# Optimization experiments

Hardware: AMD Instinct MI355X
Metric: run time of the kernel (lower is better)

The kernel has to match this reference:

```python
import jax, jax.numpy as jnp
import numpy as np

B, S, H, D = 2, 2048, 2048, 256  # batch, seq, hidden, head_dim
NH, NKV = 8, 1                   # attention heads, kv heads
N_REP = NH // NKV
SCALING = D ** -0.5
ROPE_THETA = 10000.0
NEG_INF = -1e9


def rotate_half(x):
    x1, x2 = jnp.split(x, 2, axis=-1)
    return jnp.concatenate((-x2, x1), axis=-1)


def setup_inputs() -> dict:
    key = jax.random.key(0)
    ks = jax.random.split(key, 5)
    hidden_states = jax.random.normal(ks[0], (B, S, H), dtype=jnp.float32)
    # RoPE cos/sin per position, Gemma-style: inv_freq tiled over full head_dim
    inv_freq = 1.0 / (ROPE_THETA ** (np.arange(0, D, 2, dtype=np.float32) / D))  # [D/2]
    pos = np.arange(S, dtype=np.float32)
    freqs = np.outer(pos, inv_freq)                      # [S, D/2]
    emb = np.concatenate([freqs, freqs], axis=-1)        # [S, D]
    cos = jnp.broadcast_to(jnp.asarray(np.cos(emb)), (B, S, D))
    sin = jnp.broadcast_to(jnp.asarray(np.sin(emb)), (B, S, D))
    # additive causal mask [B, 1, S, S]
    causal = jnp.triu(jnp.full((S, S), NEG_INF, dtype=jnp.float32), k=1)
    attention_mask = jnp.broadcast_to(causal[None, None], (B, 1, S, S))
    scale = 0.02
    Wq = jax.random.normal(ks[1], (H, NH * D), dtype=jnp.float32) * scale
    Wk = jax.random.normal(ks[2], (H, NKV * D), dtype=jnp.float32) * scale
    Wv = jax.random.normal(ks[3], (H, NKV * D), dtype=jnp.float32) * scale
    Wo = jax.random.normal(ks[4], (NH * D, H), dtype=jnp.float32) * scale
    return {"hidden_states": hidden_states, "cos": cos, "sin": sin,
            "attention_mask": attention_mask, "Wq": Wq, "Wk": Wk, "Wv": Wv, "Wo": Wo}


def reference(hidden_states, cos, sin, attention_mask, Wq, Wk, Wv, Wo):
    # projections: [B,S,H] @ [H, nh*D] -> [B, nh, S, D]
    q = (hidden_states @ Wq).reshape(B, S, NH, D).transpose(0, 2, 1, 3)
    k = (hidden_states @ Wk).reshape(B, S, NKV, D).transpose(0, 2, 1, 3)
    v = (hidden_states @ Wv).reshape(B, S, NKV, D).transpose(0, 2, 1, 3)
    # RoPE (cos/sin broadcast over head dim via unsqueeze at axis 1)
    c = cos[:, None]  # [B,1,S,D]
    s = sin[:, None]
    q = q * c + rotate_half(q) * s
    k = k * c + rotate_half(k) * s
    # repeat_kv: [B, NKV, S, D] -> [B, NH, S, D]
    k = jnp.repeat(k, N_REP, axis=1)
    v = jnp.repeat(v, N_REP, axis=1)
    # eager attention
    attn_weights = jnp.einsum("bhqd,bhkd->bhqk", q, k) * SCALING
    attn_weights = attn_weights + attention_mask[:, :, :, :S]
    attn_weights = jax.nn.softmax(attn_weights.astype(jnp.float32), axis=-1).astype(q.dtype)
    attn_output = jnp.einsum("bhqk,bhkd->bhqd", attn_weights, v)
    attn_output = attn_output.transpose(0, 2, 1, 3).reshape(B, S, NH * D)
    attn_output = attn_output @ Wo
    return attn_output, attn_weights
```

## Files before the change

### kernel.cpp

```cpp
#include <hip/hip_runtime.h>
#include <hip/hip_bf16.h>

#define B_   2
#define S_   2048
#define H_   2048
#define D_   256
#define NH_  8

typedef unsigned short u16;
typedef __bf16 bf16x8 __attribute__((ext_vector_type(8)));
typedef float f32x4 __attribute__((ext_vector_type(4)));
typedef unsigned int uint4v __attribute__((ext_vector_type(4)));
typedef unsigned int uint2v __attribute__((ext_vector_type(2)));

#define AS1 __attribute__((address_space(1)))
#define AS3 __attribute__((address_space(3)))

__device__ __forceinline__ u16 f2bf(float x) {
  union { float f; unsigned u; } v; v.f = x;
  unsigned u = v.u;
  u += 0x7FFFu + ((u >> 16) & 1u);
  return (u16)(u >> 16);
}
__device__ __forceinline__ float bf2f(u16 x) {
  union { unsigned u; float f; } v; v.u = ((unsigned)x) << 16;
  return v.f;
}

__device__ __forceinline__ void bf8_unpack(uint4v u, float* f) {
  f[0] = bf2f(u.x & 0xffff); f[1] = bf2f(u.x >> 16);
  f[2] = bf2f(u.y & 0xffff); f[3] = bf2f(u.y >> 16);
  f[4] = bf2f(u.z & 0xffff); f[5] = bf2f(u.z >> 16);
  f[6] = bf2f(u.w & 0xffff); f[7] = bf2f(u.w >> 16);
}
__device__ __forceinline__ uint4v bf8_pack(const float* f) {
  uint4v o;
  o.x = (unsigned)f2bf(f[0]) | ((unsigned)f2bf(f[1]) << 16);
  o.y = (unsigned)f2bf(f[2]) | ((unsigned)f2bf(f[3]) << 16);
  o.z = (unsigned)f2bf(f[4]) | ((unsigned)f2bf(f[5]) << 16);
  o.w = (unsigned)f2bf(f[6]) | ((unsigned)f2bf(f[7]) << 16);
  return o;
}

__device__ __forceinline__ void gld_lds16(const u16* g, u16* l) {
  __builtin_amdgcn_global_load_lds((const AS1 unsigned int*)g,
                                   (AS3 unsigned int*)l, 16, 0, 0);
}

#define BM 128
#define BN 128
#define BK 64

enum GemmMode { MODE_PROJ = 0, MODE_QK = 1, MODE_PV = 2, MODE_WO = 3 };

template <int MODE>
__global__ __launch_bounds__(256)
void gemm_nt(const u16* __restrict__ A, const u16* __restrict__ Bb,
             void* __restrict__ Cp, float* __restrict__ rows,
             float* __restrict__ Pout,
             int K, int lda, int ldb, int ldc)
{
  int bn, bm;
  if constexpr (MODE == MODE_QK) {
    int t = blockIdx.x;
    bm = 0;
    while ((bm + 1) * (bm + 2) / 2 <= t) bm++;
    bn = t - bm * (bm + 1) / 2;
  } else if constexpr (MODE == MODE_PV) {
    bn = blockIdx.x;
    bm = (int)gridDim.y - 1 - (int)blockIdx.y;
  } else {
    bn = blockIdx.x;
    bm = blockIdx.y;
  }
  const int bz = blockIdx.z;
  const int m0 = bm * BM, n0 = bn * BN;
  const int tid = threadIdx.x;

  const u16* Ap = A;
  const u16* Bp = Bb;
  float* Cf = (float*)Cp;
  u16*   Cu = (u16*)Cp;
  float* Pp = Pout;

  if constexpr (MODE == MODE_QK) {
    Ap   += (size_t)bz * S_ * D_;
    Bp   += (size_t)(bz >> 3) * S_ * D_;
    Cu   += (size_t)bz * S_ * S_;
    rows += (size_t)bz * S_;
  } else if constexpr (MODE == MODE_PV) {
    Ap   += (size_t)bz * S_ * S_;
    Bp   += (size_t)(bz >> 3) * D_ * S_;
    Cu   += (size_t)(bz >> 3) * S_ * (NH_ * D_) + (size_t)(bz & 7) * D_;
    rows += (size_t)bz * S_;
    Pp   += (size_t)bz * S_ * S_;
  }

  int Keff = K;
  if constexpr (MODE == MODE_PV) {
    int lim = (bm + 1) * BM;
    Keff = lim < K ? lim : K;
  }

  __shared__ __align__(16) u16 smem[BM * BK + BN * BK + 512];
  u16* As = smem;
  u16* Bs = smem + BM * BK;
  __shared__ float invs[BM];

  const int lane = tid & 63;
  const int quad = lane >> 4;
  const int l16  = lane & 15;
  const int wave = tid >> 6;
  const int wm   = (wave >> 1) << 6;
  const int wn   = (wave & 1) << 6;

  if constexpr (MODE == MODE_PV) {
    if (tid < BM) invs[tid] = 1.0f / rows[m0 + tid];
  }

  f32x4 acc[4][4] = {};

  for (int kt = 0; kt < Keff; kt += BK) {
    #pragma unroll
    for (int i = 0; i < 4; i++) {
      int c = tid + i * 256;
      gld_lds16(Ap + (size_t)(m0 + (c >> 3)) * lda + kt + (c & 7) * 8, &As[c * 8]);
    }
    #pragma unroll
    for (int i = 0; i < 4; i++) {
      int c = tid + i * 256;
      gld_lds16(Bp + (size_t)(n0 + (c >> 3)) * ldb + kt + (c & 7) * 8, &Bs[c * 8]);
    }
    __syncthreads();

    #pragma unroll
    for (int kk = 0; kk < 2; kk++) {
      bf16x8 af[4], bfr[4];
      #pragma unroll
      for (int i = 0; i < 4; i++)
        af[i] = *(const bf16x8*)(&As[(wm + i * 16 + l16) * BK + kk * 32 + quad * 8]);
      #pragma unroll
      for (int j = 0; j < 4; j++)
        bfr[j] = *(const bf16x8*)(&Bs[(wn + j * 16 + l16) * BK + kk * 32 + quad * 8]);
      #pragma unroll
      for (int i = 0; i < 4; i++)
        #pragma unroll
        for (int j = 0; j < 4; j++)
          acc[i][j] = __builtin_amdgcn_mfma_f32_16x16x32_bf16(af[i], bfr[j], acc[i][j], 0, 0, 0);
    }

    if constexpr (MODE == MODE_PV) {
      if (bn == 0) {
        const int pr4 = tid >> 4;
        const int pc4 = (tid & 15) * 4;
        #pragma unroll
        for (int rr = 0; rr < BM; rr += 16) {
          const int r = rr + pr4;
          const u16* e = &As[r * BK + pc4];
          const float inv = invs[r];
          float4 o;
          o.x = bf2f(e[0]) * inv; o.y = bf2f(e[1]) * inv;
          o.z = bf2f(e[2]) * inv; o.w = bf2f(e[3]) * inv;
          *(float4*)(Pp + (size_t)(m0 + r) * S_ + kt + pc4) = o;
        }
      }
    }
    __syncthreads();
  }

  if constexpr (MODE == MODE_PV) {
    if (bn == 0 && Keff < S_) {
      const int r8 = tid >> 3;
      const int c8 = tid & 7;
      const float4 z = {0.f, 0.f, 0.f, 0.f};
      #pragma unroll
      for (int rr = 0; rr < BM; rr += 32) {
        float* pr = Pp + (size_t)(m0 + rr + r8) * S_;
        for (int c4 = (Keff >> 2) + c8; c4 < (S_ >> 2); c4 += 8)
          *(float4*)(pr + c4 * 4) = z;
      }
    }
  }

  const float SCL2 = 0.0625f * 1.44269504088896340736f;
  if constexpr (MODE == MODE_WO) {
    float (*Cs32)[132] = (float (*)[132])smem;
    const int band16 = (wave >> 1) * 16;
    #pragma unroll
    for (int i = 0; i < 4; i++) {
      #pragma unroll
      for (int r = 0; r < 4; r++) {
        const int lr = band16 + quad * 4 + r;
        #pragma unroll
        for (int j = 0; j < 4; j++)
          Cs32[lr][wn + j * 16 + l16] = acc[i][j][r];
      }
      __syncthreads();
      #pragma unroll
      for (int ch = tid; ch < 1024; ch += 256) {
        const int rr = ch >> 5, cc = ch & 31;
        const int mg = m0 + ((rr >> 4) << 6) + i * 16 + (rr & 15);
        *(float4*)(Cf + (size_t)mg * ldc + n0 + cc * 4) =
            *(const float4*)(&Cs32[rr][cc * 4]);
      }
      __syncthreads();
    }
  } else {
    u16 (*Cs)[136] = (u16 (*)[136])smem;
    const int band16 = (wave >> 1) * 16;
    #pragma unroll
    for (int i = 0; i < 4; i++) {
      #pragma unroll
      for (int r = 0; r < 4; r++) {
        const int lr = band16 + quad * 4 + r;
        const int m  = m0 + wm + i * 16 + quad * 4 + r;
        if constexpr (MODE == MODE_QK) {
          float rs = 0.f;
          #pragma unroll
          for (int j = 0; j < 4; j++) {
            int n = n0 + wn + j * 16 + l16;
            float e = (n <= m) ? exp2f(acc[i][j][r] * SCL2) : 0.f;
            rs += e;
            Cs[lr][wn + j * 16 + l16] = f2bf(e);
          }
          #pragma unroll
          for (int o = 1; o < 16; o <<= 1) rs += __shfl_xor(rs, o, 64);
          if (l16 == 0) atomicAdd(&rows[m], rs);
        } else if constexpr (MODE == MODE_PV) {
          const float inv = invs[wm + i * 16 + quad * 4 + r];
          #pragma unroll
          for (int j = 0; j < 4; j++)
            Cs[lr][wn + j * 16 + l16] = f2bf(acc[i][j][r] * inv);
        } else {
          #pragma unroll
          for (int j = 0; j < 4; j++)
            Cs[lr][wn + j * 16 + l16] = f2bf(acc[i][j][r]);
        }
      }
      __syncthreads();
      #pragma unroll
      for (int ch = tid; ch < 512; ch += 256) {
        const int rr = ch >> 4, cc = ch & 15;
        const int mg = m0 + ((rr >> 4) << 6) + i * 16 + (rr & 15);
        *(uint4v*)(Cu + (size_t)mg * ldc + n0 + cc * 8) =
            *(const uint4v*)(&Cs[rr][cc * 8]);
      }
      __syncthreads();
    }
  }
}

__device__ __forceinline__ void tc_tile(const float* __restrict__ src,
                                        u16* __restrict__ dst, int K, int N,
                                        int n0, int k0, float (*t)[33])
{
  int c = threadIdx.x & 31, r = threadIdx.x >> 5;
  #pragma unroll
  for (int rr = 0; rr < 32; rr += 8)
    t[r + rr][c] = src[(size_t)(k0 + r + rr) * N + n0 + c];
  __syncthreads();
  #pragma unroll
  for (int rr = 0; rr < 32; rr += 8)
    dst[(size_t)(n0 + r + rr) * K + k0 + c] = f2bf(t[c][r + rr]);
}

__global__ __launch_bounds__(256)
void prep_kernel(const float* __restrict__ X,
                 const float* __restrict__ Wq, const float* __restrict__ Wk,
                 const float* __restrict__ Wv, const float* __restrict__ Wo,
                 u16* __restrict__ Xbf, u16* __restrict__ WT,
                 u16* __restrict__ WoT, float* __restrict__ Rows)
{
  __shared__ float t[32][33];
  const int bid = blockIdx.x;
  if (bid < 4096) {
    tc_tile(Wq, WT, 2048, 2048, (bid & 63) * 32, (bid >> 6) * 32, t);
  } else if (bid < 4608) {
    int l = bid - 4096;
    tc_tile(Wk, WT + 2048 * 2048, 2048, 256, (l & 7) * 32, (l >> 3) * 32, t);
  } else if (bid < 5120) {
    int l = bid - 4608;
    tc_tile(Wv, WT + 2304 * 2048, 2048, 256, (l & 7) * 32, (l >> 3) * 32, t);
  } else if (bid < 9216) {
    int l = bid - 5120;
    tc_tile(Wo, WoT, 2048, 2048, (l & 63) * 32, (l >> 6) * 32, t);
  } else if (bid < 11264) {
    int l = bid - 9216;
    #pragma unroll
    for (int it = 0; it < 4; ++it) {
      int i = it * 524288 + l * 256 + threadIdx.x;
      float4 f = ((const float4*)X)[i];
      uint2v p;
      p.x = (unsigned)f2bf(f.x) | ((unsigned)f2bf(f.y) << 16);
      p.y = (unsigned)f2bf(f.z) | ((unsigned)f2bf(f.w) << 16);
      ((uint2v*)Xbf)[i] = p;
    }
  } else {
    int l = bid - 11264;
    const float4 z = {0.f, 0.f, 0.f, 0.f};
    #pragma unroll
    for (int it = 0; it < 4; ++it)
      ((float4*)Rows)[it * 2048 + l * 256 + threadIdx.x] = z;
  }
}

__global__ __launch_bounds__(256)
void postproj_kernel(const u16* __restrict__ raw, const float* __restrict__ cosb,
                     const float* __restrict__ sinb, u16* __restrict__ qout,
                     u16* __restrict__ kout, u16* __restrict__ vt)
{
  __shared__ u16 t[32][34];
  const int bid = blockIdx.x;
  if (bid < 1024) {
    const int row = threadIdx.x >> 4;
    const int d8  = (threadIdx.x & 15) * 8;
    #pragma unroll
    for (int it2 = 0; it2 < 2; ++it2) {
      int idx = bid * 32 + it2 * 16 + row;
      int h = idx & 7, bs = idx >> 3;
      int b = bs >> 11, s = bs & (S_ - 1);
      size_t base = (size_t)bs * 2560 + (size_t)h * D_;
      uint4v u1 = *(const uint4v*)(raw + base + d8);
      uint4v u2 = *(const uint4v*)(raw + base + 128 + d8);
      float4 c0 = *(const float4*)(cosb + (size_t)bs * D_ + d8);
      float4 c1 = *(const float4*)(cosb + (size_t)bs * D_ + d8 + 4);
      float4 s0 = *(const float4*)(sinb + (size_t)bs * D_ + d8);
      float4 s1 = *(const float4*)(sinb + (size_t)bs * D_ + d8 + 4);
      float a[8], bq[8], cc[8], ss[8], r1[8], r2[8];
      bf8_unpack(u1, a); bf8_unpack(u2, bq);
      cc[0]=c0.x; cc[1]=c0.y; cc[2]=c0.z; cc[3]=c0.w;
      cc[4]=c1.x; cc[5]=c1.y; cc[6]=c1.z; cc[7]=c1.w;
      ss[0]=s0.x; ss[1]=s0.y; ss[2]=s0.z; ss[3]=s0.w;
      ss[4]=s1.x; ss[5]=s1.y; ss[6]=s1.z; ss[7]=s1.w;
      #pragma unroll
      for (int i = 0; i < 8; ++i) {
        r1[i] = a[i] * cc[i] - bq[i] * ss[i];
        r2[i] = bq[i] * cc[i] + a[i] * ss[i];
      }
      size_t ob = (((size_t)b * NH_ + h) * S_ + s) * D_;
      *(uint4v*)(qout + ob + d8)       = bf8_pack(r1);
      *(uint4v*)(qout + ob + 128 + d8) = bf8_pack(r2);
    }
  } else if (bid < 1280) {
    const int l   = bid - 1024;
    const int row = threadIdx.x >> 4;
    const int d8  = (threadIdx.x & 15) * 8;
    int bs = l * 16 + row;
    size_t base = (size_t)bs * 2560 + 2048;
    uint4v u1 = *(const uint4v*)(raw + base + d8);
    uint4v u2 = *(const uint4v*)(raw + base + 128 + d8);
    float4 c0 = *(const float4*)(cosb + (size_t)bs * D_ + d8);
    float4 c1 = *(const float4*)(cosb + (size_t)bs * D_ + d8 + 4);
    float4 s0 = *(const float4*)(sinb + (size_t)bs * D_ + d8);
    float4 s1 = *(const float4*)(sinb + (size_t)bs * D_ + d8 + 4);
    float a[8], bq[8], cc[8], ss[8], r1[8], r2[8];
    bf8_unpack(u1, a); bf8_unpack(u2, bq);
    cc[0]=c0.x; cc[1]=c0.y; cc[2]=c0.z; cc[3]=c0.w;
    cc[4]=c1.x; cc[5]=c1.y; cc[6]=c1.z; cc[7]=c1.w;
    ss[0]=s0.x; ss[1]=s0.y; ss[2]=s0.z; ss[3]=s0.w;
    ss[4]=s1.x; ss[5]=s1.y; ss[6]=s1.z; ss[7]=s1.w;
    #pragma unroll
    for (int i = 0; i < 8; ++i) {
      r1[i] = a[i] * cc[i] - bq[i] * ss[i];
      r2[i] = bq[i] * cc[i] + a[i] * ss[i];
    }
    *(uint4v*)(kout + (size_t)bs * D_ + d8)       = bf8_pack(r1);
    *(uint4v*)(kout + (size_t)bs * D_ + 128 + d8) = bf8_pack(r2);
  } else {
    int l = bid - 1280;
    int b = l >> 9, rem = l & 511;
    int d0 = (rem & 7) * 32, s0 = (rem >> 3) * 32;
    int c = threadIdx.x & 31, r = threadIdx.x >> 5;
    #pragma unroll
    for (int rr = 0; rr < 32; rr += 8)
      t[r + rr][c] = raw[(size_t)(b * S_ + s0 + r + rr) * 2560 + 2304 + d0 + c];
    __syncthreads();
    #pragma unroll
    for (int rr = 0; rr < 32; rr += 8)
      vt[(size_t)b * D_ * S_ + (size_t)(d0 + r + rr) * S_ + s0 + c] = t[c][r + rr];
  }
}

extern "C" void kernel_launch(void* const* d_in, const int* in_sizes, int n_in,
                              void* d_out, int out_size, void* d_ws, size_t ws_size,
                              hipStream_t stream)
{
  const float* X    = (const float*)d_in[0];
  const float* cosb = (const float*)d_in[1];
  const float* sinb = (const float*)d_in[2];
  const float* Wq   = (const float*)d_in[4];
  const float* Wk   = (const float*)d_in[5];
  const float* Wv   = (const float*)d_in[6];
  const float* Wo   = (const float*)d_in[7];

  float* outO = (float*)d_out;
  float* outP = outO + (size_t)B_ * S_ * H_;

  u16* ws     = (u16*)d_ws;
  u16* Xbf    = ws;
  u16* WT     = Xbf    + 8388608;
  u16* WoT    = WT     + 5242880;
  u16* QKVraw = WoT    + 4194304;
  u16* Qbf    = QKVraw + 10485760;
  u16* Kbf    = Qbf    + 8388608;
  u16* VT     = Kbf    + 1048576;
  u16* AObf   = VT     + 1048576;
  u16* Ebf    = AObf   + 8388608;
  float* Rows = (float*)(Ebf + 67108864);

  prep_kernel<<<11272, 256, 0, stream>>>(X, Wq, Wk, Wv, Wo, Xbf, WT, WoT, Rows);
  gemm_nt<MODE_PROJ><<<dim3(20, 32, 1), 256, 0, stream>>>(
      Xbf, WT, QKVraw, nullptr, nullptr, 2048, 2048, 2048, 2560);
  postproj_kernel<<<2304, 256, 0, stream>>>(QKVraw, cosb, sinb, Qbf, Kbf, VT);
  gemm_nt<MODE_QK><<<dim3(136, 1, 16), 256, 0, stream>>>(
      Qbf, Kbf, Ebf, Rows, nullptr, 256, 256, 256, 2048);
  gemm_nt<MODE_PV><<<dim3(2, 16, 16), 256, 0, stream>>>(
      Ebf, VT, AObf, Rows, outP, 2048, 2048, 2048, 2048);
  gemm_nt<MODE_WO><<<dim3(16, 32, 1), 256, 0, stream>>>(
      AObf, WoT, outO, nullptr, nullptr, 2048, 2048, 2048, 2048);
}
```

Before: 665.2 us.

## Halve GEMM K-tile, swizzle block order per XCD, relax PV barrier

Shrinks the K tile from 64 to 32, which halves LDS use per block and can allow more resident blocks, at the cost of twice as many barriers per K loop. The projection and output GEMMs now use a 1D grid whose block index is remapped round-robin across the 8 XCDs, so blocks that share operands tend to run on the same XCD and reuse its L2. The PV mode replaces the trailing __syncthreads with an LDS-only wait plus s_barrier, and its probability write-out is rewritten to read packed 32-bit values from LDS. The smaller tile lowers arithmetic intensity per synchronization and may hurt MFMA throughput.

```diff
diff --git a/kernel.cpp b/kernel.cpp
--- a/kernel.cpp
+++ b/kernel.cpp
@@ -49,7 +49,7 @@
 
 #define BM 128
 #define BN 128
-#define BK 64
+#define BK 32
 
 enum GemmMode { MODE_PROJ = 0, MODE_QK = 1, MODE_PV = 2, MODE_WO = 3 };
 
@@ -58,7 +58,7 @@
 void gemm_nt(const u16* __restrict__ A, const u16* __restrict__ Bb,
              void* __restrict__ Cp, float* __restrict__ rows,
              float* __restrict__ Pout,
-             int K, int lda, int ldb, int ldc)
+             int K, int lda, int ldb, int ldc, int nx)
 {
   int bn, bm;
   if constexpr (MODE == MODE_QK) {
@@ -70,8 +70,11 @@
     bn = blockIdx.x;
     bm = (int)gridDim.y - 1 - (int)blockIdx.y;
   } else {
-    bn = blockIdx.x;
-    bm = blockIdx.y;
+    int orig = blockIdx.x;
+    int cpx  = (int)gridDim.x >> 3;
+    int swz  = (orig & 7) * cpx + (orig >> 3);
+    bm = swz / nx;
+    bn = swz - bm * nx;
   }
   const int bz = blockIdx.z;
   const int m0 = bm * BM, n0 = bn * BN;
@@ -122,50 +125,49 @@
 
   for (int kt = 0; kt < Keff; kt += BK) {
     #pragma unroll
-    for (int i = 0; i < 4; i++) {
+    for (int i = 0; i < 2; i++) {
       int c = tid + i * 256;
-      gld_lds16(Ap + (size_t)(m0 + (c >> 3)) * lda + kt + (c & 7) * 8, &As[c * 8]);
-    }
-    #pragma unroll
-    for (int i = 0; i < 4; i++) {
+      gld_lds16(Ap + (size_t)(m0 + (c >> 2)) * lda + kt + (c & 3) * 8, &As[c * 8]);
+    }
+    #pragma unroll
+    for (int i = 0; i < 2; i++) {
       int c = tid + i * 256;
-      gld_lds16(Bp + (size_t)(n0 + (c >> 3)) * ldb + kt + (c & 7) * 8, &Bs[c * 8]);
+      gld_lds16(Bp + (size_t)(n0 + (c >> 2)) * ldb + kt + (c & 3) * 8, &Bs[c * 8]);
     }
     __syncthreads();
 
-    #pragma unroll
-    for (int kk = 0; kk < 2; kk++) {
-      bf16x8 af[4], bfr[4];
-      #pragma unroll
-      for (int i = 0; i < 4; i++)
-        af[i] = *(const bf16x8*)(&As[(wm + i * 16 + l16) * BK + kk * 32 + quad * 8]);
+    bf16x8 af[4], bfr[4];
+    #pragma unroll
+    for (int i = 0; i < 4; i++)
+      af[i] = *(const bf16x8*)(&As[(wm + i * 16 + l16) * BK + quad * 8]);
+    #pragma unroll
+    for (int j = 0; j < 4; j++)
+      bfr[j] = *(const bf16x8*)(&Bs[(wn + j * 16 + l16) * BK + quad * 8]);
+    #pragma unroll
+    for (int i = 0; i < 4; i++)
       #pragma unroll
       for (int j = 0; j < 4; j++)
-        bfr[j] = *(const bf16x8*)(&Bs[(wn + j * 16 + l16) * BK + kk * 32 + quad * 8]);
-      #pragma unroll
-      for (int i = 0; i < 4; i++)
-        #pragma unroll
-        for (int j = 0; j < 4; j++)
-          acc[i][j] = __builtin_amdgcn_mfma_f32_16x16x32_bf16(af[i], bfr[j], acc[i][j], 0, 0, 0);
-    }
+        acc[i][j] = __builtin_amdgcn_mfma_f32_16x16x32_bf16(af[i], bfr[j], acc[i][j], 0, 0, 0);
 
     if constexpr (MODE == MODE_PV) {
       if (bn == 0) {
-        const int pr4 = tid >> 4;
-        const int pc4 = (tid & 15) * 4;
+        const int r8 = tid >> 3;
+        const int c8 = tid & 7;
         #pragma unroll
-        for (int rr = 0; rr < BM; rr += 16) {
-          const int r = rr + pr4;
-          const u16* e = &As[r * BK + pc4];
+        for (int rr = 0; rr < BM; rr += 32) {
+          const int r = rr + r8;
+          uint2v u = *(const uint2v*)(&As[r * BK + c8 * 4]);
           const float inv = invs[r];
           float4 o;
-          o.x = bf2f(e[0]) * inv; o.y = bf2f(e[1]) * inv;
-          o.z = bf2f(e[2]) * inv; o.w = bf2f(e[3]) * inv;
-          *(float4*)(Pp + (size_t)(m0 + r) * S_ + kt + pc4) = o;
+          o.x = bf2f(u.x & 0xffff) * inv; o.y = bf2f(u.x >> 16) * inv;
+          o.z = bf2f(u.y & 0xffff) * inv; o.w = bf2f(u.y >> 16) * inv;
+          *(float4*)(Pp + (size_t)(m0 + r) * S_ + kt + c8 * 4) = o;
         }
       }
-    }
-    __syncthreads();
+      asm volatile("s_waitcnt lgkmcnt(0)\n\ts_barrier" ::: "memory");
+    } else {
+      __syncthreads();
+    }
   }
 
   if constexpr (MODE == MODE_PV) {
@@ -409,13 +411,13 @@
   float* Rows = (float*)(Ebf + 67108864);
 
   prep_kernel<<<11272, 256, 0, stream>>>(X, Wq, Wk, Wv, Wo, Xbf, WT, WoT, Rows);
-  gemm_nt<MODE_PROJ><<<dim3(20, 32, 1), 256, 0, stream>>>(
-      Xbf, WT, QKVraw, nullptr, nullptr, 2048, 2048, 2048, 2560);
+  gemm_nt<MODE_PROJ><<<640, 256, 0, stream>>>(
+      Xbf, WT, QKVraw, nullptr, nullptr, 2048, 2048, 2048, 2560, 20);
   postproj_kernel<<<2304, 256, 0, stream>>>(QKVraw, cosb, sinb, Qbf, Kbf, VT);
   gemm_nt<MODE_QK><<<dim3(136, 1, 16), 256, 0, stream>>>(
-      Qbf, Kbf, Ebf, Rows, nullptr, 256, 256, 256, 2048);
+      Qbf, Kbf, Ebf, Rows, nullptr, 256, 256, 256, 2048, 0);
   gemm_nt<MODE_PV><<<dim3(2, 16, 16), 256, 0, stream>>>(
-      Ebf, VT, AObf, Rows, outP, 2048, 2048, 2048, 2048);
-  gemm_nt<MODE_WO><<<dim3(16, 32, 1), 256, 0, stream>>>(
-      AObf, WoT, outO, nullptr, nullptr, 2048, 2048, 2048, 2048);
-}
+      Ebf, VT, AObf, Rows, outP, 2048, 2048, 2048, 2048, 0);
+  gemm_nt<MODE_WO><<<512, 256, 0, stream>>>(
+      AObf, WoT, outO, nullptr, nullptr, 2048, 2048, 2048, 2048, 16);
+}
```

Result: faster. 637.5 us (-4.2%).
